# Optimization experiments

Hardware: AMD Instinct MI355X
Metric: run time of the kernel (lower is better)

The kernel has to match this reference:

```python
import jax, jax.numpy as jnp
import numpy as np

INPUT_DIM = 1024
OUTPUT_DIM = 1024
DEGREE = 8
N_TOKENS = 8192


def setup_inputs() -> dict:
    key = jax.random.key(0)
    k1, k2 = jax.random.split(key)
    x = jax.random.normal(k1, (N_TOKENS, INPUT_DIM), dtype=jnp.float32)
    # xavier_normal_ with gain = 1/(input_dim*(degree+1)) over fan dims (output_dim, degree+1)
    fan_in, fan_out = OUTPUT_DIM, DEGREE + 1  # torch treats dim0/dim1 as fans; scale is tiny anyway
    gain = 1.0 / (INPUT_DIM * (DEGREE + 1))
    std = gain * np.sqrt(2.0 / (INPUT_DIM + OUTPUT_DIM))
    cheby_coeffs = std * jax.random.normal(k2, (INPUT_DIM, OUTPUT_DIM, DEGREE + 1), dtype=jnp.float32)
    return {"x": x, "cheby_coeffs": cheby_coeffs}


def reference(x, cheby_coeffs):
    # x: (..., input_dim) -> y: (..., output_dim)
    degree_p1 = cheby_coeffs.shape[-1]
    theta = jnp.arccos(jnp.tanh(x))                      # (..., i)
    arange = jnp.arange(degree_p1, dtype=x.dtype)        # (d,)
    basis = jnp.cos(theta[..., None] * arange)           # (..., i, d) Chebyshev T_d(tanh(x))
    y = jnp.einsum('...id,iod->...o', basis, cheby_coeffs)
    return y
```

## Files before the change

kernel.cpp:

```cpp
#include <hip/hip_runtime.h>


typedef __bf16 bf16;
typedef __bf16 bf16x8 __attribute__((ext_vector_type(8)));
typedef float f32x2 __attribute__((ext_vector_type(2)));
typedef float f32x4 __attribute__((ext_vector_type(4)));
typedef float f32x16 __attribute__((ext_vector_type(16)));

#define MFMA __builtin_amdgcn_mfma_f32_32x32x16_bf16

__device__ __forceinline__ void g2lds16(const void* g, void* l) {
  __builtin_amdgcn_global_load_lds(
      (const __attribute__((address_space(1))) unsigned int*)g,
      (__attribute__((address_space(3))) unsigned int*)l, 16, 0, 0);
}

__device__ __forceinline__ float fast_tanh(float a) {
  float e = __expf(a + a);
  return 1.f - 2.f * __builtin_amdgcn_rcpf(e + 1.f);
}

__global__ __launch_bounds__(256)
void cheby_prepB(const float* __restrict__ C, bf16* __restrict__ B,
                 float* __restrict__ bias_p) {
  const int b2 = blockIdx.x, tid = threadIdx.x;
  __shared__ float tile[32][292];
  const int i0 = (b2 >> 5) * 32, o0 = (b2 & 31) * 32;
  {
    const int r = tid >> 3, seg = tid & 7;
    const float* src = C + (size_t)(i0 + r) * 9216 + (size_t)o0 * 9 + seg * 36;
    float* dst = &tile[r][seg * 36];
    #pragma unroll
    for (int v = 0; v < 9; ++v) *(f32x4*)(dst + v * 4) = *(const f32x4*)(src + v * 4);
  }
  __syncthreads();
  #pragma unroll
  for (int j = 0; j < 4; ++j) {
    int e = tid + 256 * j;
    int il = e >> 5, ol = e & 31;
    int i = i0 + il, o = o0 + ol;
    bf16x8 v;
    #pragma unroll
    for (int d = 0; d < 8; ++d) v[d] = (bf16)tile[il][ol * 9 + 1 + d];
    const int cc = i & 7;
    size_t tnum = (size_t)(o >> 7) * 128 + (i >> 3);
    const int widx = (((cc >> 1) * 4 + ((o & 127) >> 5)) * 2 + (cc & 1)) * 32 + (o & 31);
    *(bf16x8*)(B + tnum * 8192 + widx * 8) = v;
  }
  if (tid < 32) {
    float s = 0.f;
    #pragma unroll
    for (int i = 0; i < 32; ++i) s += tile[i][tid * 9];
    bias_p[(size_t)(b2 >> 5) * 1024 + o0 + tid] = s;
  }
}

__global__ __launch_bounds__(256)
void cheby_prepT(const float* __restrict__ x, float* __restrict__ th2) {
  const int bid = blockIdx.x, tid = threadIdx.x;
  __shared__ float xs[64][129];
  const int r0 = (bid >> 3) * 64, c0 = (bid & 7) * 128;
  #pragma unroll
  for (int it = 0; it < 8; ++it) {
    const int e = tid + it * 256;
    const int rr = e >> 5, c4 = (e & 31) * 4;
    f32x4 v = *(const f32x4*)(x + (size_t)(r0 + rr) * 1024 + c0 + c4);
    xs[rr][c4 + 0] = v.x; xs[rr][c4 + 1] = v.y;
    xs[rr][c4 + 2] = v.z; xs[rr][c4 + 3] = v.w;
  }
  __syncthreads();
  const int row = tid & 63, kq = tid >> 6;
  const int mt = r0 >> 7, rowp = (r0 & 127) + row;
  const int kt0 = c0 >> 3;
  float* outp = th2 + (size_t)mt * 131072;
  #pragma unroll
  for (int kk = 0; kk < 4; ++kk) {
    const int kt = kq * 4 + kk;
    #pragma unroll
    for (int li = 0; li < 8; ++li) {
      float z = fast_tanh(xs[row][kt * 8 + li]);
      const int pos = (li & 1) * 4 + (li >> 1);
      outp[(size_t)(kt0 + kt) * 1024 + pos * 128 + rowp] = z;
    }
  }
}

__global__ __launch_bounds__(256, 2)
void cheby_gemm9(const float* __restrict__ th2, const bf16* __restrict__ B,
                 const float* __restrict__ bias_p, float* __restrict__ out) {
  __shared__ bf16 ring[3][10240];
  const int tid = threadIdx.x;
  const int lane = tid & 63, w = tid >> 6;
  const int wm = w >> 1, wn = w & 1;
  const int bid = blockIdx.x;
  const int wgid = (bid & 7) * 64 + (bid >> 3);
  const int mt = wgid >> 3, nb = wgid & 7;

  const int ml = lane & 31, h = lane >> 5;
  const int bBase = wn * 1024 + h * 256 + ml * 8;
  const int sBase = h * 512 + wm * 64 + ml;

  const bf16*  bG = B   + (size_t)nb * 1048576 + tid * 8;
  const float* tG = th2 + (size_t)mt * 131072 + tid * 4;

  f32x16 acc[2][2];
  #pragma unroll
  for (int a = 0; a < 2; ++a)
    #pragma unroll
    for (int b = 0; b < 2; ++b)
      #pragma unroll
      for (int r = 0; r < 16; ++r) acc[a][b][r] = 0.f;

  auto issue5 = [&](int t, int p) {
    #pragma unroll
    for (int c = 0; c < 4; ++c)
      g2lds16(bG + (size_t)t * 8192 + c * 2048, &ring[p][c * 2048 + tid * 8]);
    g2lds16(tG + (size_t)t * 1024, &ring[p][8192 + tid * 8]);
  };

  issue5(0, 0); issue5(1, 1);
  asm volatile("s_waitcnt vmcnt(5)" ::: "memory");
  __builtin_amdgcn_s_barrier();

  auto step = [&](int t, int pC, int pN) {
    if (t + 2 < 128) issue5(t + 2, pN);
    const bf16* ra = &ring[pC][0];
    const float* seedL = (const float*)(ra + 8192);
    bf16x8 bfr[2][4], afr[2][4];
    #pragma unroll
    for (int ks = 0; ks < 4; ++ks) {
      bfr[0][ks] = *(const bf16x8*)(ra + bBase + ks * 2048);
      bfr[1][ks] = *(const bf16x8*)(ra + bBase + ks * 2048 + 512);
    }
    #pragma unroll
    for (int ks = 0; ks < 4; ++ks) {
      f32x2 tv = { seedL[sBase + ks * 128], seedL[sBase + ks * 128 + 32] };
      f32x2 t2 = tv + tv;
      f32x2 prev = {1.f, 1.f}, cur = tv;
      #pragma unroll
      for (int j = 0; j < 8; ++j) {
        afr[0][ks][j] = (bf16)cur.x;
        afr[1][ks][j] = (bf16)cur.y;
        f32x2 nx = t2 * cur - prev;
        prev = cur; cur = nx;
      }
    }
    __builtin_amdgcn_s_setprio(1);
    #pragma unroll
    for (int ks = 0; ks < 4; ++ks) {
      acc[0][0] = MFMA(afr[0][ks], bfr[0][ks], acc[0][0], 0, 0, 0);
      acc[0][1] = MFMA(afr[0][ks], bfr[1][ks], acc[0][1], 0, 0, 0);
      acc[1][0] = MFMA(afr[1][ks], bfr[0][ks], acc[1][0], 0, 0, 0);
      acc[1][1] = MFMA(afr[1][ks], bfr[1][ks], acc[1][1], 0, 0, 0);
    }
    __builtin_amdgcn_s_setprio(0);
    asm volatile("s_waitcnt lgkmcnt(0)" ::: "memory");
    if (t <= 125) asm volatile("s_waitcnt vmcnt(5)" ::: "memory");
    else          asm volatile("s_waitcnt vmcnt(0)" ::: "memory");
    __builtin_amdgcn_s_barrier();
  };

  #pragma unroll 1
  for (int t3 = 0; t3 < 126; t3 += 3) {
    step(t3,     0, 2);
    step(t3 + 1, 1, 0);
    step(t3 + 2, 2, 1);
  }
  step(126, 0, 2);
  step(127, 1, 0);

  const int c0 = nb * 128 + wn * 64 + ml;
  float bv0 = 0.f, bv1 = 0.f;
  #pragma unroll
  for (int p = 0; p < 32; ++p) {
    bv0 += bias_p[(size_t)p * 1024 + c0];
    bv1 += bias_p[(size_t)p * 1024 + c0 + 32];
  }
  const int r0 = mt * 128 + wm * 64;
  #pragma unroll
  for (int mtt = 0; mtt < 2; ++mtt)
    #pragma unroll
    for (int r = 0; r < 16; ++r) {
      int row = r0 + mtt * 32 + (r & 3) + 8 * (r >> 2) + 4 * h;
      float* po = out + (size_t)row * 1024 + c0;
      po[0]  = acc[mtt][0][r] + bv0;
      po[32] = acc[mtt][1][r] + bv1;
    }
}

__global__ __launch_bounds__(256)
void cheby_naive(const float* __restrict__ x, const float* __restrict__ C,
                 float* __restrict__ out) {
  const int t = blockIdx.x, tid = threadIdx.x;
  float acc[4] = {0.f, 0.f, 0.f, 0.f};
  for (int i = 0; i < 1024; ++i) {
    float th = tanhf(x[(size_t)t * 1024 + i]);
    float T[9]; T[0] = 1.f; T[1] = th;
    #pragma unroll
    for (int d = 2; d < 9; ++d) T[d] = 2.f * th * T[d - 1] - T[d - 2];
    #pragma unroll
    for (int j = 0; j < 4; ++j) {
      const float* cp = &C[((size_t)i * 1024 + tid + j * 256) * 9];
      float s = 0.f;
      #pragma unroll
      for (int d = 0; d < 9; ++d) s += T[d] * cp[d];
      acc[j] += s;
    }
  }
  #pragma unroll
  for (int j = 0; j < 4; ++j) out[(size_t)t * 1024 + tid + j * 256] = acc[j];
}

extern "C" void kernel_launch(void* const* d_in, const int* in_sizes, int n_in,
                              void* d_out, int out_size, void* d_ws, size_t ws_size,
                              hipStream_t stream) {
  (void)in_sizes; (void)n_in; (void)out_size;
  const float* x = (const float*)d_in[0];
  const float* C = (const float*)d_in[1];
  float* out = (float*)d_out;

  const size_t b_bytes  = (size_t)8 * 128 * 8192 * 2;
  const size_t bp_bytes = (size_t)32 * 1024 * 4;
  const size_t th_bytes = (size_t)64 * 128 * 1024 * 4;

  if (ws_size >= b_bytes + bp_bytes + th_bytes) {
    bf16*  B      = (bf16*)d_ws;
    float* bias_p = (float*)((char*)d_ws + b_bytes);
    float* th2    = (float*)((char*)d_ws + b_bytes + bp_bytes);
    cheby_prepB<<<1024, 256, 0, stream>>>(C, B, bias_p);
    cheby_prepT<<<1024, 256, 0, stream>>>(x, th2);
    cheby_gemm9<<<512, 256, 0, stream>>>(th2, B, bias_p, out);
  } else {
    cheby_naive<<<8192, 256, 0, stream>>>(x, C, out);
  }
}
```

Baseline: 255.4 us.

## Merge prep kernels and store tanh in row-major layout for direct GEMM loads

Folds the tanh preprocessing and the coefficient repacking into one launch, removing a kernel launch and its gap. The tanh pass no longer transposes through LDS: each thread reads eight contiguous x values and writes them back row-major, reordered even/odd. The GEMM now loads 16-byte row chunks of the seed tile and reads each lane's seeds as two 16-byte LDS vectors instead of eight scalar loads. The risk is that the new global-to-LDS pattern gathers from 128 separate rows per tile, so the GEMM's loads are less coalesced.

```diff
diff --git a/kernel.cpp b/kernel.cpp
--- a/kernel.cpp
+++ b/kernel.cpp
@@ -21,9 +21,23 @@
 }
 
 __global__ __launch_bounds__(256)
-void cheby_prepB(const float* __restrict__ C, bf16* __restrict__ B,
-                 float* __restrict__ bias_p) {
-  const int b2 = blockIdx.x, tid = threadIdx.x;
+void cheby_prep7(const float* __restrict__ x, const float* __restrict__ C,
+                 bf16* __restrict__ B, float* __restrict__ bias_p,
+                 float* __restrict__ th2) {
+  const int bid = blockIdx.x, tid = threadIdx.x;
+  if (bid < 4096) {
+    const size_t g = (size_t)bid * 256 + tid;
+    const float* xp = x + g * 8;
+    f32x4 a  = *(const f32x4*)(xp);
+    f32x4 b4 = *(const f32x4*)(xp + 4);
+    f32x4 e = { fast_tanh(a.x), fast_tanh(a.z), fast_tanh(b4.x), fast_tanh(b4.z) };
+    f32x4 o = { fast_tanh(a.y), fast_tanh(a.w), fast_tanh(b4.y), fast_tanh(b4.w) };
+    float* dp = th2 + g * 8;
+    *(f32x4*)dp       = e;
+    *(f32x4*)(dp + 4) = o;
+    return;
+  }
+  const int b2 = bid - 4096;
   __shared__ float tile[32][292];
   const int i0 = (b2 >> 5) * 32, o0 = (b2 & 31) * 32;
   {
@@ -55,39 +69,9 @@
   }
 }
 
-__global__ __launch_bounds__(256)
-void cheby_prepT(const float* __restrict__ x, float* __restrict__ th2) {
-  const int bid = blockIdx.x, tid = threadIdx.x;
-  __shared__ float xs[64][129];
-  const int r0 = (bid >> 3) * 64, c0 = (bid & 7) * 128;
-  #pragma unroll
-  for (int it = 0; it < 8; ++it) {
-    const int e = tid + it * 256;
-    const int rr = e >> 5, c4 = (e & 31) * 4;
-    f32x4 v = *(const f32x4*)(x + (size_t)(r0 + rr) * 1024 + c0 + c4);
-    xs[rr][c4 + 0] = v.x; xs[rr][c4 + 1] = v.y;
-    xs[rr][c4 + 2] = v.z; xs[rr][c4 + 3] = v.w;
-  }
-  __syncthreads();
-  const int row = tid & 63, kq = tid >> 6;
-  const int mt = r0 >> 7, rowp = (r0 & 127) + row;
-  const int kt0 = c0 >> 3;
-  float* outp = th2 + (size_t)mt * 131072;
-  #pragma unroll
-  for (int kk = 0; kk < 4; ++kk) {
-    const int kt = kq * 4 + kk;
-    #pragma unroll
-    for (int li = 0; li < 8; ++li) {
-      float z = fast_tanh(xs[row][kt * 8 + li]);
-      const int pos = (li & 1) * 4 + (li >> 1);
-      outp[(size_t)(kt0 + kt) * 1024 + pos * 128 + rowp] = z;
-    }
-  }
-}
-
 __global__ __launch_bounds__(256, 2)
-void cheby_gemm9(const float* __restrict__ th2, const bf16* __restrict__ B,
-                 const float* __restrict__ bias_p, float* __restrict__ out) {
+void cheby_gemm10(const float* __restrict__ th2, const bf16* __restrict__ B,
+                  const float* __restrict__ bias_p, float* __restrict__ out) {
   __shared__ bf16 ring[3][10240];
   const int tid = threadIdx.x;
   const int lane = tid & 63, w = tid >> 6;
@@ -98,10 +82,10 @@
 
   const int ml = lane & 31, h = lane >> 5;
   const int bBase = wn * 1024 + h * 256 + ml * 8;
-  const int sBase = h * 512 + wm * 64 + ml;
-
-  const bf16*  bG = B   + (size_t)nb * 1048576 + tid * 8;
-  const float* tG = th2 + (size_t)mt * 131072 + tid * 4;
+  const int sB = (wm * 64 + ml) * 8 + h * 4;
+
+  const bf16*  bG = B + (size_t)nb * 1048576 + tid * 8;
+  const float* tG = th2 + (size_t)(mt * 128 + (tid >> 1)) * 1024 + (tid & 1) * 4;
 
   f32x16 acc[2][2];
   #pragma unroll
@@ -115,7 +99,7 @@
     #pragma unroll
     for (int c = 0; c < 4; ++c)
       g2lds16(bG + (size_t)t * 8192 + c * 2048, &ring[p][c * 2048 + tid * 8]);
-    g2lds16(tG + (size_t)t * 1024, &ring[p][8192 + tid * 8]);
+    g2lds16(tG + t * 8, &ring[p][8192 + tid * 8]);
   };
 
   issue5(0, 0); issue5(1, 1);
@@ -132,9 +116,11 @@
       bfr[0][ks] = *(const bf16x8*)(ra + bBase + ks * 2048);
       bfr[1][ks] = *(const bf16x8*)(ra + bBase + ks * 2048 + 512);
     }
+    f32x4 s0 = *(const f32x4*)(seedL + sB);
+    f32x4 s1 = *(const f32x4*)(seedL + sB + 256);
     #pragma unroll
     for (int ks = 0; ks < 4; ++ks) {
-      f32x2 tv = { seedL[sBase + ks * 128], seedL[sBase + ks * 128 + 32] };
+      f32x2 tv = { s0[ks], s1[ks] };
       f32x2 t2 = tv + tv;
       f32x2 prev = {1.f, 1.f}, cur = tv;
       #pragma unroll
@@ -221,15 +207,14 @@
 
   const size_t b_bytes  = (size_t)8 * 128 * 8192 * 2;
   const size_t bp_bytes = (size_t)32 * 1024 * 4;
-  const size_t th_bytes = (size_t)64 * 128 * 1024 * 4;
+  const size_t th_bytes = (size_t)8192 * 1024 * 4;
 
   if (ws_size >= b_bytes + bp_bytes + th_bytes) {
     bf16*  B      = (bf16*)d_ws;
     float* bias_p = (float*)((char*)d_ws + b_bytes);
     float* th2    = (float*)((char*)d_ws + b_bytes + bp_bytes);
-    cheby_prepB<<<1024, 256, 0, stream>>>(C, B, bias_p);
-    cheby_prepT<<<1024, 256, 0, stream>>>(x, th2);
-    cheby_gemm9<<<512, 256, 0, stream>>>(th2, B, bias_p, out);
+    cheby_prep7<<<5120, 256, 0, stream>>>(x, C, B, bias_p, th2);
+    cheby_gemm10<<<512, 256, 0, stream>>>(th2, B, bias_p, out);
   } else {
     cheby_naive<<<8192, 256, 0, stream>>>(x, C, out);
   }
```

Result: no change. 257.2 us (+0.7%).
